# Optimization experiments

Hardware: AMD Instinct MI355X
Metric: run time of the kernel (lower is better)

The kernel has to match this reference:

```python
import jax, jax.numpy as jnp
import numpy as np

N = 100000      # nodes
E = 800000      # edges (nnz of sparse adj)
D_IN = 128      # input feature dim
H = 64          # hidden_units
EMB = 32        # embsize
N_IDX = 50000   # gathered output rows
EPS = 1e-05     # BatchNormalization epsilon


def spmm(rows, cols, vals, x):
    # out[i] = sum_{e: rows[e]==i} vals[e] * x[cols[e]]  == sparse A @ x
    return jax.ops.segment_sum(vals[:, None] * x[cols], rows, num_segments=N)


def batchnorm(x, gamma, beta):
    # training-mode BN over node (batch) axis, matching Keras BatchNormalization
    m = jnp.mean(x, axis=0)
    v = jnp.var(x, axis=0)
    return (x - m) * jax.lax.rsqrt(v + EPS) * gamma + beta


def setup_inputs() -> dict:
    key = jax.random.key(0)
    ks = jax.random.split(key, 16)
    def w(k, fan_in, shape):
        return jax.random.normal(k, shape, dtype=jnp.float32) / np.sqrt(fan_in)
    inp = {
        "features": jax.random.normal(ks[0], (N, D_IN), dtype=jnp.float32),
        "rows": jax.random.randint(ks[1], (E,), 0, N),
        "cols": jax.random.randint(ks[2], (E,), 0, N),
        "vals": jax.random.uniform(ks[3], (E,), dtype=jnp.float32),
        "idx": jax.random.randint(ks[4], (N_IDX,), 0, N),
        # layer 0 (Dense with bias since l==0)
        "Wn0": w(ks[5], D_IN, (D_IN, H)), "bn0": jnp.zeros((H,), jnp.float32),
        "Wg0": w(ks[6], D_IN, (D_IN, H)), "bg0": jnp.zeros((H,), jnp.float32),
        "ab0": jnp.zeros((H,), jnp.float32),  # BiasLayer after SpMM
        "g0": jnp.ones((H,), jnp.float32), "b0": jnp.zeros((H,), jnp.float32),
        # layer 1 (no Dense bias)
        "Wn1": w(ks[7], H, (H, H)),
        "Wg1": w(ks[8], H, (H, H)),
        "ab1": jnp.zeros((H,), jnp.float32),
        "g1": jnp.ones((H,), jnp.float32), "b1": jnp.zeros((H,), jnp.float32),
        # conv_last block (Dense use_bias=False)
        "WnL": w(ks[9], H, (H, EMB)),
        "WgL": w(ks[10], H, (H, EMB)),
        "abL": jnp.zeros((EMB,), jnp.float32),
    }
    return inp


def reference(features, rows, cols, vals, idx,
              Wn0, bn0, Wg0, bg0, ab0, g0, b0,
              Wn1, Wg1, ab1, g1, b1,
              WnL, WgL, abL):
    x = features
    # SAGE layer 0
    x_node = x @ Wn0 + bn0
    x_neigh = x @ Wg0 + bg0
    agg = spmm(rows, cols, vals, x_neigh) + ab0
    x = jax.nn.relu(batchnorm(x_node + agg, g0, b0))
    # SAGE layer 1
    x_node = x @ Wn1
    x_neigh = x @ Wg1
    agg = spmm(rows, cols, vals, x_neigh) + ab1
    x = jax.nn.relu(batchnorm(x_node + agg, g1, b1))
    # conv_last projection to embsize
    x_node = x @ WnL
    x_neigh = x @ WgL
    agg = spmm(rows, cols, vals, x_neigh) + abL
    x = x_node + agg
    return x[idx]
```

## Files before the change

kernel.cpp:

```cpp
#include <hip/hip_runtime.h>

#define NNODES 100000
#define NEDGES 800000
#define DIN    128
#define HID    64
#define EMB    32
#define NIDX   50000
#define BN_EPS 1e-5f

#define NCHK 64
#define EC   (NEDGES / NCHK)
#define SUBC 256
#define ECS  (NEDGES / SUBC)
#define NB   ((NNODES + 63) / 64)

typedef __attribute__((ext_vector_type(8))) short short8;
typedef __attribute__((ext_vector_type(4))) float f32x4;

__device__ inline unsigned short f2bf(float f) {
    unsigned u = __float_as_uint(f);
    unsigned r = u + 0x7FFFu + ((u >> 16) & 1u);
    return (unsigned short)(r >> 16);
}
__device__ inline float bf2f_lo(unsigned u) { return __uint_as_float(u << 16); }
__device__ inline float bf2f_hi(unsigned u) { return __uint_as_float(u & 0xffff0000u); }


__device__ inline void pack_seg(const float* __restrict__ Wn, const float* __restrict__ Wg,
                                unsigned short* __restrict__ Wp, int HOUT, int l2nt, int f) {
    int j = f & 7, lane = (f >> 3) & 63, g = f >> 9;
    int tt = g & ((1 << l2nt) - 1), kb = g >> l2nt;
    int k = kb * 32 + ((lane >> 4) * 8) + j;
    int nn = tt * 16 + (lane & 15);
    float v = (nn < HOUT) ? Wn[k * HOUT + nn] : Wg[k * HOUT + (nn - HOUT)];
    Wp[f] = f2bf(v);
}

__global__ void packall_k(const float* Wn0, const float* Wg0, const float* Wn1,
                          const float* Wg1, const float* WnL, const float* WgL,
                          unsigned short* Wp0, unsigned short* Wp1, unsigned short* WpL) {
    int f = blockIdx.x * 256 + threadIdx.x;
    if (f < 16384)      pack_seg(Wn0, Wg0, Wp0, 64, 3, f);
    else if (f < 24576) pack_seg(Wn1, Wg1, Wp1, 64, 3, f - 16384);
    else if (f < 28672) pack_seg(WnL, WgL, WpL, 32, 2, f - 24576);
}


__global__ __launch_bounds__(256) void bhist_k(const int* __restrict__ rows,
                                               int* __restrict__ Bcnt4,
                                               const int* __restrict__ idx,
                                               int* __restrict__ mark) {
    if ((int)blockIdx.x >= SUBC) {
        int j = ((int)blockIdx.x - SUBC) * 256 + threadIdx.x;
        if (j < NIDX) mark[idx[j]] = 1;
        return;
    }
    __shared__ int hist[NB];
    int t = threadIdx.x, blk = blockIdx.x;
    for (int b = t; b < NB; b += 256) hist[b] = 0;
    __syncthreads();
    for (int i = t; i < ECS; i += 256)
        atomicAdd(&hist[rows[blk * ECS + i] >> 6], 1);
    __syncthreads();
    for (int b = t; b < NB; b += 256) Bcnt4[blk * NB + b] = hist[b];
}

__global__ void bprefix_k(const int* __restrict__ Bcnt4, int* __restrict__ BcntT,
                          int* __restrict__ bTot) {
    int b = blockIdx.x * 256 + threadIdx.x;
    if (b >= NB) return;
    int run = 0;
    for (int sub = 0; sub < SUBC; sub++) {
        if ((sub & 3) == 0) BcntT[(sub >> 2) * NB + b] = run;
        run += Bcnt4[sub * NB + b];
    }
    bTot[b] = run;
}

__global__ void bscan_k(const int* __restrict__ bTot, int* __restrict__ bBase) {
    __shared__ int s[256];
    int t = threadIdx.x;
    int v[7], loc = 0;
#pragma unroll
    for (int i = 0; i < 7; i++) {
        int ix = t * 7 + i;
        v[i] = loc;
        loc += (ix < NB) ? bTot[ix] : 0;
    }
    s[t] = loc;
    __syncthreads();
    for (int off = 1; off < 256; off <<= 1) {
        int a = (t >= off) ? s[t - off] : 0;
        __syncthreads();
        s[t] += a;
        __syncthreads();
    }
    int base = s[t] - loc;
#pragma unroll
    for (int i = 0; i < 7; i++) {
        int ix = t * 7 + i;
        if (ix < NB) bBase[ix] = base + v[i];
    }
    if (t == 255) bBase[NB] = NEDGES;
}

__global__ __launch_bounds__(256) void bfinal_k(const int4* __restrict__ ebuf,
                                                const int* __restrict__ bBase,
                                                int* __restrict__ rowptr,
                                                int2* __restrict__ cs) {
    __shared__ int hist[64], sc[64], cur[64];
    int b = blockIdx.x, t = threadIdx.x;
    int e0 = bBase[b], e1 = bBase[b + 1];
    int r0 = b << 6;
    if (t < 64) hist[t] = 0;
    __syncthreads();
    for (int i = e0 + t; i < e1; i += 256)
        atomicAdd(&hist[ebuf[i].x & 63], 1);
    __syncthreads();
    if (t == 0) {
        int run = e0;
        for (int j = 0; j < 64; j++) { sc[j] = run; run += hist[j]; }
    }
    __syncthreads();
    if (t < 64) {
        cur[t] = sc[t];
        int r = r0 + t;
        if (r < NNODES) rowptr[r] = sc[t];
    }
    if (b == NB - 1 && t == 0) rowptr[NNODES] = NEDGES;
    __syncthreads();
    for (int i = e0 + t; i < e1; i += 256) {
        int4 v = ebuf[i];
        int p = atomicAdd(&cur[v.x & 63], 1);
        cs[p] = make_int2(v.y, v.z);
    }
}


template <int K, int HOUT, bool AFF, bool XBF, bool HNBF>
__device__ void gemm_body(const void* __restrict__ Xv, const unsigned short* __restrict__ Wp,
                          const float* __restrict__ bnA, const float* __restrict__ bnB,
                          const float* __restrict__ bgA,
                          const float* __restrict__ sums, const float* __restrict__ gamma,
                          const float* __restrict__ beta,
                          float* __restrict__ Hnf, unsigned short* __restrict__ Hnb,
                          unsigned short* __restrict__ Hgb, int n, int blk)
{
    constexpr int NT = 2 * HOUT / 16, NKB = K / 32;
    constexpr int RS = K + 8;
    __shared__ unsigned short Xs[64 * RS];
    __shared__ float sSc[64], sSh[64];

    const int row0 = blk * 64;
    const int t = threadIdx.x;

    if (AFF) {
        if (t < 64) {
            float sum = 0.f, sq = 0.f;
#pragma unroll
            for (int s = 0; s < 8; s++) { sum += sums[s * 128 + t]; sq += sums[s * 128 + 64 + t]; }
            float m = sum / (float)NNODES;
            float var = sq / (float)NNODES - m * m;
            float sc = gamma[t] * rsqrtf(var + BN_EPS);
            sSc[t] = sc; sSh[t] = beta[t] - m * sc;
        }
        __syncthreads();
    }

    for (int li = t; li < 64 * K / 8; li += 256) {
        int r  = li / (K / 8);
        int k8 = (li % (K / 8)) * 8;
        int rr = row0 + r;
        float v[8];
        if (XBF) {
            uint4 u = (rr < n) ? *(const uint4*)((const unsigned short*)Xv + (size_t)rr * K + k8)
                               : make_uint4(0, 0, 0, 0);
            v[0] = bf2f_lo(u.x); v[1] = bf2f_hi(u.x);
            v[2] = bf2f_lo(u.y); v[3] = bf2f_hi(u.y);
            v[4] = bf2f_lo(u.z); v[5] = bf2f_hi(u.z);
            v[6] = bf2f_lo(u.w); v[7] = bf2f_hi(u.w);
        } else {
            const float* Xf = (const float*)Xv;
            float4 a = make_float4(0.f, 0.f, 0.f, 0.f), b = a;
            if (rr < n) {
                a = *(const float4*)&Xf[(size_t)rr * K + k8];
                b = *(const float4*)&Xf[(size_t)rr * K + k8 + 4];
            }
            v[0] = a.x; v[1] = a.y; v[2] = a.z; v[3] = a.w;
            v[4] = b.x; v[5] = b.y; v[6] = b.z; v[7] = b.w;
        }
        if (AFF) {
#pragma unroll
            for (int i = 0; i < 8; i++) v[i] = fmaxf(v[i] * sSc[k8 + i] + sSh[k8 + i], 0.f);
        }
        uint4 o;
        o.x = (unsigned)f2bf(v[0]) | ((unsigned)f2bf(v[1]) << 16);
        o.y = (unsigned)f2bf(v[2]) | ((unsigned)f2bf(v[3]) << 16);
        o.z = (unsigned)f2bf(v[4]) | ((unsigned)f2bf(v[5]) << 16);
        o.w = (unsigned)f2bf(v[6]) | ((unsigned)f2bf(v[7]) << 16);
        *(uint4*)&Xs[r * RS + k8] = o;
    }
    __syncthreads();

    const int wave = t >> 6, lane = t & 63;
    const int q = lane >> 4, mrow = lane & 15;

    f32x4 acc[NT];
#pragma unroll
    for (int i = 0; i < NT; i++) acc[i] = (f32x4){0.f, 0.f, 0.f, 0.f};

    const short8* wp8 = (const short8*)Wp;
#pragma unroll
    for (int kb = 0; kb < NKB; kb++) {
        short8 a = *(const short8*)&Xs[(wave * 16 + mrow) * RS + kb * 32 + q * 8];
#pragma unroll
        for (int tt = 0; tt < NT; tt++) {
            short8 b = wp8[(kb * NT + tt) * 64 + lane];
            acc[tt] = __builtin_amdgcn_mfma_f32_16x16x32_bf16(a, b, acc[tt], 0, 0, 0);
        }
    }

#pragma unroll
    for (int tt = 0; tt < NT; tt++) {
        int nglob = tt * 16 + mrow;
        bool nside = (nglob < HOUT);
        int c = nside ? nglob : (nglob - HOUT);
        float bias = 0.f;
        if (nside) {
            if (bnA) bias += bnA[c];
            if (bnB) bias += bnB[c];
        } else if (bgA) {
            bias += bgA[c];
        }
#pragma unroll
        for (int r = 0; r < 4; r++) {
            int rr = row0 + wave * 16 + q * 4 + r;
            if (rr < n) {
                float o = acc[tt][r] + bias;
                if (nside) {
                    if (HNBF) Hnb[(size_t)rr * HOUT + c] = f2bf(o);
                    else      Hnf[(size_t)rr * HOUT + c] = o;
                } else {
                    Hgb[(size_t)rr * HOUT + c] = f2bf(o);
                }
            }
        }
    }
}

__global__ __launch_bounds__(256) void part_gemm0_k(
    const int* __restrict__ rows, const int* __restrict__ cols,
    const float* __restrict__ vals, const int* __restrict__ BcntT,
    const int* __restrict__ bBase, int4* __restrict__ ebuf,
    const float* __restrict__ X, const unsigned short* __restrict__ Wp0,
    const float* __restrict__ bn0, const float* __restrict__ ab0, const float* __restrict__ bg0,
    unsigned short* __restrict__ Hn0b, unsigned short* __restrict__ Hgb, int n)
{
    if ((int)blockIdx.x < NCHK) {
        __shared__ int cur[NB];
        int t = threadIdx.x, blk = blockIdx.x;
        for (int b = t; b < NB; b += 256) cur[b] = bBase[b] + BcntT[blk * NB + b];
        __syncthreads();
        for (int i = t; i < EC; i += 256) {
            int e = blk * EC + i;
            int r = rows[e];
            int p = atomicAdd(&cur[r >> 6], 1);
            ebuf[p] = make_int4(r, cols[e], __float_as_int(vals[e]), 0);
        }
    } else {
        gemm_body<DIN, HID, false, false, true>(X, Wp0, bn0, ab0, bg0,
            nullptr, nullptr, nullptr, nullptr, Hn0b, Hgb, n, blockIdx.x - NCHK);
    }
}

template <int K, int HOUT, bool AFF, bool XBF, bool HNBF>
__global__ __launch_bounds__(256) void gemm_k(
    const void* __restrict__ X, const unsigned short* __restrict__ Wp,
    const float* __restrict__ bnA, const float* __restrict__ bnB, const float* __restrict__ bgA,
    const float* __restrict__ sums, const float* __restrict__ gamma, const float* __restrict__ beta,
    float* __restrict__ Hnf, unsigned short* __restrict__ Hnb, unsigned short* __restrict__ Hgb, int n)
{
    gemm_body<K, HOUT, AFF, XBF, HNBF>(X, Wp, bnA, bnB, bgA, sums, gamma, beta,
                                       Hnf, Hnb, Hgb, n, blockIdx.x);
}


template <int HH, bool STATS, bool SBF, bool MARKED>
__global__ __launch_bounds__(256) void spmm_k(
    const int* __restrict__ rowptr, const int2* __restrict__ cs,
    const unsigned short* __restrict__ Hgb, void* __restrict__ Sv,
    float* __restrict__ stats, const int* __restrict__ mark, int n)
{
    constexpr int L  = HH / 4;
    constexpr int GP = 256 / L;
    const int lane = threadIdx.x % L;
    const int g = threadIdx.x / L;
    const int gid = blockIdx.x * GP + g;
    const int ngroups = gridDim.x * GP;
    const int c0 = lane * 4;

    float4 sum = make_float4(0.f, 0.f, 0.f, 0.f);
    float4 sq  = make_float4(0.f, 0.f, 0.f, 0.f);
    for (int row = gid; row < n; row += ngroups) {
        if (MARKED && !mark[row]) continue;
        int e0 = rowptr[row], e1 = rowptr[row + 1];
        float4 a0, a1 = make_float4(0.f, 0.f, 0.f, 0.f);
        if (SBF) {
            uint2 h = *(const uint2*)((const unsigned short*)Sv + (size_t)row * HH + c0);
            a0 = make_float4(bf2f_lo(h.x), bf2f_hi(h.x), bf2f_lo(h.y), bf2f_hi(h.y));
        } else {
            a0 = *(const float4*)((const float*)Sv + (size_t)row * HH + c0);
        }
        int e = e0;
        for (; e + 1 < e1; e += 2) {
            int2 p0 = cs[e], p1 = cs[e + 1];
            float v0 = __int_as_float(p0.y), v1 = __int_as_float(p1.y);
            uint2 h0 = *(const uint2*)&Hgb[(size_t)p0.x * HH + c0];
            uint2 h1 = *(const uint2*)&Hgb[(size_t)p1.x * HH + c0];
            a0.x += v0 * bf2f_lo(h0.x); a0.y += v0 * bf2f_hi(h0.x);
            a0.z += v0 * bf2f_lo(h0.y); a0.w += v0 * bf2f_hi(h0.y);
            a1.x += v1 * bf2f_lo(h1.x); a1.y += v1 * bf2f_hi(h1.x);
            a1.z += v1 * bf2f_lo(h1.y); a1.w += v1 * bf2f_hi(h1.y);
        }
        if (e < e1) {
            int2 p = cs[e];
            float v = __int_as_float(p.y);
            uint2 h = *(const uint2*)&Hgb[(size_t)p.x * HH + c0];
            a0.x += v * bf2f_lo(h.x); a0.y += v * bf2f_hi(h.x);
            a0.z += v * bf2f_lo(h.y); a0.w += v * bf2f_hi(h.y);
        }
        float4 acc = make_float4(a0.x + a1.x, a0.y + a1.y, a0.z + a1.z, a0.w + a1.w);
        if (SBF) {
            uint2 o;
            o.x = (unsigned)f2bf(acc.x) | ((unsigned)f2bf(acc.y) << 16);
            o.y = (unsigned)f2bf(acc.z) | ((unsigned)f2bf(acc.w) << 16);
            *(uint2*)((unsigned short*)Sv + (size_t)row * HH + c0) = o;
        } else {
            *(float4*)((float*)Sv + (size_t)row * HH + c0) = acc;
        }
        if (STATS) {
            sum.x += acc.x; sum.y += acc.y; sum.z += acc.z; sum.w += acc.w;
            sq.x += acc.x * acc.x; sq.y += acc.y * acc.y;
            sq.z += acc.z * acc.z; sq.w += acc.w * acc.w;
        }
    }

    if constexpr (STATS) {
        __shared__ float rs[GP][HH];
        __shared__ float rq[GP][HH];
        *(float4*)&rs[g][c0] = sum;
        *(float4*)&rq[g][c0] = sq;
        __syncthreads();
        if (threadIdx.x < HH) {
            float a = 0.f, b = 0.f;
            for (int w = 0; w < GP; w++) { a += rs[w][threadIdx.x]; b += rq[w][threadIdx.x]; }
            int stripe = blockIdx.x & 7;
            atomicAdd(&stats[stripe * 128 + threadIdx.x], a);
            atomicAdd(&stats[stripe * 128 + HH + threadIdx.x], b);
        }
    }
}

__global__ void gather_k(const float* __restrict__ S, const int* __restrict__ idx,
                         float* __restrict__ out, int total4) {
    int j = blockIdx.x * 256 + threadIdx.x;
    if (j < total4) {
        int r = j / (EMB / 4), c4 = (j % (EMB / 4)) * 4;
        *(float4*)&out[(size_t)j * 4] = *(const float4*)&S[(size_t)idx[r] * EMB + c4];
    }
}


extern "C" void kernel_launch(void* const* d_in, const int* in_sizes, int n_in,
                              void* d_out, int out_size, void* d_ws, size_t ws_size,
                              hipStream_t stream) {
    const float* features = (const float*)d_in[0];
    const int*   rows     = (const int*)d_in[1];
    const int*   cols     = (const int*)d_in[2];
    const float* vals     = (const float*)d_in[3];
    const int*   idx      = (const int*)d_in[4];
    const float* Wn0 = (const float*)d_in[5];
    const float* bn0 = (const float*)d_in[6];
    const float* Wg0 = (const float*)d_in[7];
    const float* bg0 = (const float*)d_in[8];
    const float* ab0 = (const float*)d_in[9];
    const float* g0  = (const float*)d_in[10];
    const float* b0  = (const float*)d_in[11];
    const float* Wn1 = (const float*)d_in[12];
    const float* Wg1 = (const float*)d_in[13];
    const float* ab1 = (const float*)d_in[14];
    const float* g1  = (const float*)d_in[15];
    const float* b1  = (const float*)d_in[16];
    const float* WnL = (const float*)d_in[17];
    const float* WgL = (const float*)d_in[18];
    const float* abL = (const float*)d_in[19];
    float* out = (float*)d_out;

    float*          HnLf = (float*)d_ws;
    unsigned short* nA   = (unsigned short*)(HnLf + (size_t)NNODES * EMB);
    unsigned short* nB   = nA + (size_t)NNODES * HID;
    unsigned short* Hgb  = nB + (size_t)NNODES * HID;
    int4*  ebuf  = (int4*)(Hgb + (size_t)NNODES * HID);
    int2*  cs    = (int2*)(ebuf + NEDGES);
    int*   rowptr = (int*)(cs + NEDGES);
    int*   Bcnt4 = rowptr + (NNODES + 4);
    int*   BcntT = Bcnt4 + SUBC * NB;
    int*   bTot  = BcntT + NCHK * NB;
    int*   bBase = bTot + 1568;
    unsigned short* Wp0 = (unsigned short*)(bBase + 1568);
    unsigned short* Wp1 = Wp0 + 16384;
    unsigned short* WpL = Wp1 + 8192;
    float* stats = (float*)(WpL + 4096);
    int*   mark  = (int*)(stats + 2304);
    float* sums0 = stats;
    float* sums1 = stats + 1024;
    size_t zbytes = 2304 * 4 + (size_t)NNODES * 4;

    hipMemsetAsync(stats, 0, zbytes, stream);

    const int GBm = (NNODES + 63) / 64;
    const int MB  = (NIDX + 255) / 256;

    packall_k<<<112, 256, 0, stream>>>(Wn0, Wg0, Wn1, Wg1, WnL, WgL, Wp0, Wp1, WpL);

    bhist_k<<<SUBC + MB, 256, 0, stream>>>(rows, Bcnt4, idx, mark);
    bprefix_k<<<7, 256, 0, stream>>>(Bcnt4, BcntT, bTot);
    bscan_k<<<1, 256, 0, stream>>>(bTot, bBase);
    part_gemm0_k<<<NCHK + GBm, 256, 0, stream>>>(rows, cols, vals, BcntT, bBase, ebuf,
                                                 features, Wp0, bn0, ab0, bg0,
                                                 nA, Hgb, NNODES);
    bfinal_k<<<NB, 256, 0, stream>>>(ebuf, bBase, rowptr, cs);

    spmm_k<HID, true, true, false><<<1600, 256, 0, stream>>>(rowptr, cs, Hgb, nA, sums0, nullptr, NNODES);

    gemm_k<HID, HID, true, true, true><<<GBm, 256, 0, stream>>>(
        nA, Wp1, ab1, nullptr, nullptr, sums0, g0, b0, nullptr, nB, Hgb, NNODES);
    spmm_k<HID, true, true, false><<<1600, 256, 0, stream>>>(rowptr, cs, Hgb, nB, sums1, nullptr, NNODES);

    gemm_k<HID, EMB, true, true, false><<<GBm, 256, 0, stream>>>(
        nB, WpL, abL, nullptr, nullptr, sums1, g1, b1, HnLf, nullptr, Hgb, NNODES);
    spmm_k<EMB, false, false, true><<<1600, 256, 0, stream>>>(rowptr, cs, Hgb, HnLf, nullptr, mark, NNODES);

    gather_k<<<(NIDX * EMB / 4 + 255) / 256, 256, 0, stream>>>(HnLf, idx, out, NIDX * EMB / 4);
}
```

Baseline: 303.0 us.

## Pack edge buffer to 8 bytes, fuse weight packing into histogram, more scatter chunks

Packs the intermediate edge buffer entries from int4 into uint2, holding the local row in the high bits and the column in the low 20 bits, which halves the scatter and read traffic. Merges the weight-packing kernel into the histogram kernel to remove one launch. Raises the scatter partition count to 256 chunks, using the per-subchunk prefix directly, for more parallelism. The bit packing relies on node ids fitting in 20 bits.

```diff
diff --git a/kernel.cpp b/kernel.cpp
--- a/kernel.cpp
+++ b/kernel.cpp
@@ -8,7 +8,7 @@
 #define NIDX   50000
 #define BN_EPS 1e-5f
 
-#define NCHK 64
+#define NCHK 256
 #define EC   (NEDGES / NCHK)
 #define SUBC 256
 #define ECS  (NEDGES / SUBC)
@@ -36,27 +36,29 @@
     Wp[f] = f2bf(v);
 }
 
-__global__ void packall_k(const float* Wn0, const float* Wg0, const float* Wn1,
-                          const float* Wg1, const float* WnL, const float* WgL,
-                          unsigned short* Wp0, unsigned short* Wp1, unsigned short* WpL) {
-    int f = blockIdx.x * 256 + threadIdx.x;
-    if (f < 16384)      pack_seg(Wn0, Wg0, Wp0, 64, 3, f);
-    else if (f < 24576) pack_seg(Wn1, Wg1, Wp1, 64, 3, f - 16384);
-    else if (f < 28672) pack_seg(WnL, WgL, WpL, 32, 2, f - 24576);
-}
-
-
-__global__ __launch_bounds__(256) void bhist_k(const int* __restrict__ rows,
-                                               int* __restrict__ Bcnt4,
-                                               const int* __restrict__ idx,
-                                               int* __restrict__ mark) {
-    if ((int)blockIdx.x >= SUBC) {
-        int j = ((int)blockIdx.x - SUBC) * 256 + threadIdx.x;
+
+__global__ __launch_bounds__(256) void histpack_k(
+    const int* __restrict__ rows, int* __restrict__ Bcnt4,
+    const int* __restrict__ idx, int* __restrict__ mark,
+    const float* Wn0, const float* Wg0, const float* Wn1,
+    const float* Wg1, const float* WnL, const float* WgL,
+    unsigned short* Wp0, unsigned short* Wp1, unsigned short* WpL, int MB)
+{
+    int blk = blockIdx.x;
+    if (blk >= SUBC + MB) {
+        int f = (blk - SUBC - MB) * 256 + threadIdx.x;
+        if (f < 16384)      pack_seg(Wn0, Wg0, Wp0, 64, 3, f);
+        else if (f < 24576) pack_seg(Wn1, Wg1, Wp1, 64, 3, f - 16384);
+        else if (f < 28672) pack_seg(WnL, WgL, WpL, 32, 2, f - 24576);
+        return;
+    }
+    if (blk >= SUBC) {
+        int j = (blk - SUBC) * 256 + threadIdx.x;
         if (j < NIDX) mark[idx[j]] = 1;
         return;
     }
     __shared__ int hist[NB];
-    int t = threadIdx.x, blk = blockIdx.x;
+    int t = threadIdx.x;
     for (int b = t; b < NB; b += 256) hist[b] = 0;
     __syncthreads();
     for (int i = t; i < ECS; i += 256)
@@ -71,7 +73,7 @@
     if (b >= NB) return;
     int run = 0;
     for (int sub = 0; sub < SUBC; sub++) {
-        if ((sub & 3) == 0) BcntT[(sub >> 2) * NB + b] = run;
+        BcntT[sub * NB + b] = run;
         run += Bcnt4[sub * NB + b];
     }
     bTot[b] = run;
@@ -104,7 +106,7 @@
     if (t == 255) bBase[NB] = NEDGES;
 }
 
-__global__ __launch_bounds__(256) void bfinal_k(const int4* __restrict__ ebuf,
+__global__ __launch_bounds__(256) void bfinal_k(const uint2* __restrict__ ebuf,
                                                 const int* __restrict__ bBase,
                                                 int* __restrict__ rowptr,
                                                 int2* __restrict__ cs) {
@@ -115,7 +117,7 @@
     if (t < 64) hist[t] = 0;
     __syncthreads();
     for (int i = e0 + t; i < e1; i += 256)
-        atomicAdd(&hist[ebuf[i].x & 63], 1);
+        atomicAdd(&hist[(ebuf[i].x >> 20) & 63], 1);
     __syncthreads();
     if (t == 0) {
         int run = e0;
@@ -130,9 +132,9 @@
     if (b == NB - 1 && t == 0) rowptr[NNODES] = NEDGES;
     __syncthreads();
     for (int i = e0 + t; i < e1; i += 256) {
-        int4 v = ebuf[i];
-        int p = atomicAdd(&cur[v.x & 63], 1);
-        cs[p] = make_int2(v.y, v.z);
+        uint2 v = ebuf[i];
+        int p = atomicAdd(&cur[(v.x >> 20) & 63], 1);
+        cs[p] = make_int2((int)(v.x & 0xFFFFF), (int)v.y);
     }
 }
 
@@ -251,7 +253,7 @@
 __global__ __launch_bounds__(256) void part_gemm0_k(
     const int* __restrict__ rows, const int* __restrict__ cols,
     const float* __restrict__ vals, const int* __restrict__ BcntT,
-    const int* __restrict__ bBase, int4* __restrict__ ebuf,
+    const int* __restrict__ bBase, uint2* __restrict__ ebuf,
     const float* __restrict__ X, const unsigned short* __restrict__ Wp0,
     const float* __restrict__ bn0, const float* __restrict__ ab0, const float* __restrict__ bg0,
     unsigned short* __restrict__ Hn0b, unsigned short* __restrict__ Hgb, int n)
@@ -265,7 +267,8 @@
             int e = blk * EC + i;
             int r = rows[e];
             int p = atomicAdd(&cur[r >> 6], 1);
-            ebuf[p] = make_int4(r, cols[e], __float_as_int(vals[e]), 0);
+            ebuf[p] = make_uint2(((unsigned)(r & 63) << 20) | (unsigned)cols[e],
+                                 (unsigned)__float_as_int(vals[e]));
         }
     } else {
         gemm_body<DIN, HID, false, false, true>(X, Wp0, bn0, ab0, bg0,
@@ -400,7 +403,7 @@
     unsigned short* nA   = (unsigned short*)(HnLf + (size_t)NNODES * EMB);
     unsigned short* nB   = nA + (size_t)NNODES * HID;
     unsigned short* Hgb  = nB + (size_t)NNODES * HID;
-    int4*  ebuf  = (int4*)(Hgb + (size_t)NNODES * HID);
+    uint2* ebuf  = (uint2*)(Hgb + (size_t)NNODES * HID);
     int2*  cs    = (int2*)(ebuf + NEDGES);
     int*   rowptr = (int*)(cs + NEDGES);
     int*   Bcnt4 = rowptr + (NNODES + 4);
@@ -421,9 +424,8 @@
     const int GBm = (NNODES + 63) / 64;
     const int MB  = (NIDX + 255) / 256;
 
-    packall_k<<<112, 256, 0, stream>>>(Wn0, Wg0, Wn1, Wg1, WnL, WgL, Wp0, Wp1, WpL);
-
-    bhist_k<<<SUBC + MB, 256, 0, stream>>>(rows, Bcnt4, idx, mark);
+    histpack_k<<<SUBC + MB + 112, 256, 0, stream>>>(
+        rows, Bcnt4, idx, mark, Wn0, Wg0, Wn1, Wg1, WnL, WgL, Wp0, Wp1, WpL, MB);
     bprefix_k<<<7, 256, 0, stream>>>(Bcnt4, BcntT, bTot);
     bscan_k<<<1, 256, 0, stream>>>(bTot, bBase);
     part_gemm0_k<<<NCHK + GBm, 256, 0, stream>>>(rows, cols, vals, BcntT, bBase, ebuf,
```

New measurement: 282.6 us. 6.7% less time.
